# Kernel optimization log

Measured on AMD Instinct MI355X. Metric: run time of the kernel, lower is better.

The kernel has to match this reference:

```python
import jax, jax.numpy as jnp
import numpy as np

UNITS = 256
LB = -17.0
UB = 8.0
STEP = 0.05
NUM_BUCKETS = int((UB - LB) / STEP) + 1  # 501
RESIDUE = LB - STEP
W_INIT = 0.5
BATCH = 65536


def setup_inputs() -> dict:
    key = jax.random.key(0)
    kx, = jax.random.split(key, 1)
    x = jax.random.normal(kx, (BATCH, UNITS), dtype=jnp.float32)
    v = jnp.ones((UNITS, NUM_BUCKETS), dtype=jnp.float32) * W_INIT
    b = jnp.zeros((UNITS,), dtype=jnp.float32)
    return {"x": x, "v": v, "b": b}


def reference(x, v, b):
    # x: (batch, units); v: (units, num_buckets); b: (units,)
    x_clipped = jnp.clip(x, LB + 1e-9, UB - 1e-9)
    indx = ((x_clipped - LB + STEP) / STEP).astype(jnp.int32)
    indx = jnp.clip(indx, 0, NUM_BUCKETS - 1)  # (batch, units)
    delta = x_clipped - LB + STEP - indx.astype(x.dtype) * STEP

    w = jax.nn.relu(v)  # (units, num_buckets)
    # exclusive cumsum over buckets: csum[u, j] = sum_{k<j} w[u, k]
    csum = jnp.cumsum(w, axis=1)
    csum = jnp.concatenate([jnp.zeros((w.shape[0], 1), w.dtype), csum[:, :-1]], axis=1)

    unit_idx = jnp.arange(UNITS)[None, :]  # (1, units) broadcasts with indx
    csum_g = csum[unit_idx, indx]  # (batch, units)
    w_g = w[unit_idx, indx]        # (batch, units)

    # Equivalent to sum over buckets of (triangular step mask + scattered delta) * relu(v)
    logits = STEP * csum_g + delta * w_g + RESIDUE + b[None, :]
    return jax.nn.sigmoid(logits)
```

## Files before the change

kernel.cpp:

```cpp
#include <hip/hip_runtime.h>

#define UNITS 256
#define NB 501
#define NBA 502
#define STEPF 0.05f
#define LBF -17.0f
#define UBF 8.0f
#define RESIDUEF -17.05f
#define LOG2E 1.4426950408889634f

#define WLO 208
#define WSZ 224
#define UPB 32
#define PADF 225
#define THREADS 1024
#define ROWS_PB 2048
#define CHUNKS 16
#define RD 3

typedef float floatx4 __attribute__((ext_vector_type(4)));

__global__ __launch_bounds__(256) void build_table_kernel(
    const float* __restrict__ v, const float* __restrict__ b,
    float* __restrict__ gtab) {
  const int lane = threadIdx.x & 63;
  const int wave = threadIdx.x >> 6;
  const int u = blockIdx.x * 4 + wave;
  if (u >= UNITS) return;

  const float* vu = v + u * NB;
  float pref[8];
  float run = 0.0f;
#pragma unroll
  for (int k = 0; k < 8; ++k) {
    const int j = lane * 8 + k;
    const float wv = (j < NB) ? fmaxf(vu[j], 0.0f) : 0.0f;
    pref[k] = run;
    run += wv;
  }
  float s = run;
#pragma unroll
  for (int d = 1; d < 64; d <<= 1) {
    const float o = __shfl_up(s, d, 64);
    if (lane >= d) s += o;
  }
  const float base = s - run;
  const float off = RESIDUEF + b[u];
#pragma unroll
  for (int k = 0; k < 8; ++k) {
    const int j = lane * 8 + k;
    if (j < NBA) {
      gtab[u * NBA + j] = (STEPF * (base + pref[k]) + off) * LOG2E;
    }
  }
}

__global__ __launch_bounds__(THREADS, 8) void iso_main_kernel(
    const float* __restrict__ x, const float* __restrict__ gtab,
    float* __restrict__ out) {
  __shared__ float tab[UPB * PADF];

  const int bu = blockIdx.x & 7;
  const int bb = blockIdx.x >> 3;
  const int u0 = bu * UPB;
  const int tid = threadIdx.x;

  {
    const int ul = tid >> 5;
    const int jt = tid & 31;
    const float* __restrict__ src = gtab + (u0 + ul) * NBA + WLO;
    float* __restrict__ dst = tab + ul * PADF;
#pragma unroll
    for (int r = 0; r < 7; ++r) {
      const int j = jt + r * 32;
      dst[j] = src[j];
    }
    if (jt == 0) dst[224] = src[224];
  }

  const int rowoff = tid >> 3;
  const int col4 = tid & 7;
  const floatx4* __restrict__ x4 = reinterpret_cast<const floatx4*>(x);
  floatx4* __restrict__ o4 = reinterpret_cast<floatx4*>(out);
  const int g0 = (bb * ROWS_PB + rowoff) * (UNITS / 4) + bu * (UPB / 4) + col4;
  const int gstep = 128 * (UNITS / 4);
  const int qrow = col4 * 4;

  __syncthreads();

  floatx4 xv[4];
#pragma unroll
  for (int c = 0; c < RD; ++c) xv[c] = x4[g0 + c * gstep];
  __builtin_amdgcn_sched_barrier(0);

#pragma unroll
  for (int c = 0; c < CHUNKS; ++c) {
    if (c + RD < CHUNKS)
      xv[(c + RD) & 3] = x4[g0 + (c + RD) * gstep];
    __builtin_amdgcn_sched_barrier(0);

    const floatx4 cur = xv[c & 3];
    const float xs[4] = {cur.x, cur.y, cur.z, cur.w};
    float os[4];
#pragma unroll
    for (int k = 0; k < 4; ++k) {
      const float xc = fminf(fmaxf(xs[k], LBF + 1e-9f), UBF - 1e-9f);
      const float t = xc - LBF + STEPF;
      const float ft = t * 20.0f;
      const int idx = (int)ft;
      const float f = ft - (float)idx;
      const unsigned iw = (unsigned)(idx - WLO);
      float a0, a1;
      if (iw < WSZ) {
        const float* p = &tab[(qrow + k) * PADF + (int)iw];
        a0 = p[0];
        a1 = p[1];
      } else {
        const int ci = idx < 1 ? 1 : (idx > NB - 1 ? NB - 1 : idx);
        const float* g = gtab + (u0 + qrow + k) * NBA + ci;
        a0 = g[0];
        a1 = g[1];
      }
      const float l2 = fmaf(f, a1 - a0, a0);
      const float e = __builtin_amdgcn_exp2f(-l2);
      os[k] = __builtin_amdgcn_rcpf(1.0f + e);
    }
    floatx4 ov;
    ov.x = os[0]; ov.y = os[1]; ov.z = os[2]; ov.w = os[3];
    __builtin_nontemporal_store(ov, &o4[g0 + c * gstep]);
    __builtin_amdgcn_sched_barrier(0);
  }
}

extern "C" void kernel_launch(void* const* d_in, const int* in_sizes, int n_in,
                              void* d_out, int out_size, void* d_ws,
                              size_t ws_size, hipStream_t stream) {
  const float* x = (const float*)d_in[0];
  const float* v = (const float*)d_in[1];
  const float* b = (const float*)d_in[2];
  float* out = (float*)d_out;
  float* gtab = (float*)d_ws;

  build_table_kernel<<<64, 256, 0, stream>>>(v, b, gtab);

  const int rows = out_size / UNITS;
  const int grid = (UNITS / UPB) * (rows / ROWS_PB);
  iso_main_kernel<<<grid, THREADS, 0, stream>>>(x, gtab, out);
}
```

Baseline: 131.7 us.

## Fuse table build into main kernel with full per-unit LDS table

Drops the separate table-building kernel. Each block now computes the prefix-sum logit table for its 32 units directly into shared memory, holding the full 502-entry table instead of a 224-entry window with a global fallback, which removes the branch and the global gather. Rows per block are halved to 1024 and the x prefetch depth is raised, with the first x loads issued before the barrier so they overlap table construction. In exchange every block recomputes the table from v, shared memory per block roughly doubles, and the grid doubles.

```diff
diff --git a/kernel.cpp b/kernel.cpp
--- a/kernel.cpp
+++ b/kernel.cpp
@@ -9,73 +9,57 @@
 #define RESIDUEF -17.05f
 #define LOG2E 1.4426950408889634f
 
-#define WLO 208
-#define WSZ 224
 #define UPB 32
-#define PADF 225
+#define PADF 503
 #define THREADS 1024
-#define ROWS_PB 2048
-#define CHUNKS 16
-#define RD 3
+#define ROWS_PB 1024
+#define CHUNKS 8
+#define RD 5
 
 typedef float floatx4 __attribute__((ext_vector_type(4)));
 
-__global__ __launch_bounds__(256) void build_table_kernel(
-    const float* __restrict__ v, const float* __restrict__ b,
-    float* __restrict__ gtab) {
-  const int lane = threadIdx.x & 63;
-  const int wave = threadIdx.x >> 6;
-  const int u = blockIdx.x * 4 + wave;
-  if (u >= UNITS) return;
-
-  const float* vu = v + u * NB;
-  float pref[8];
-  float run = 0.0f;
-#pragma unroll
-  for (int k = 0; k < 8; ++k) {
-    const int j = lane * 8 + k;
-    const float wv = (j < NB) ? fmaxf(vu[j], 0.0f) : 0.0f;
-    pref[k] = run;
-    run += wv;
-  }
-  float s = run;
-#pragma unroll
-  for (int d = 1; d < 64; d <<= 1) {
-    const float o = __shfl_up(s, d, 64);
-    if (lane >= d) s += o;
-  }
-  const float base = s - run;
-  const float off = RESIDUEF + b[u];
-#pragma unroll
-  for (int k = 0; k < 8; ++k) {
-    const int j = lane * 8 + k;
-    if (j < NBA) {
-      gtab[u * NBA + j] = (STEPF * (base + pref[k]) + off) * LOG2E;
-    }
-  }
-}
-
 __global__ __launch_bounds__(THREADS, 8) void iso_main_kernel(
-    const float* __restrict__ x, const float* __restrict__ gtab,
-    float* __restrict__ out) {
+    const float* __restrict__ x, const float* __restrict__ v,
+    const float* __restrict__ b, float* __restrict__ out) {
   __shared__ float tab[UPB * PADF];
 
   const int bu = blockIdx.x & 7;
   const int bb = blockIdx.x >> 3;
   const int u0 = bu * UPB;
   const int tid = threadIdx.x;
+  const int lane = tid & 63;
+  const int wv = tid >> 6;
 
-  {
-    const int ul = tid >> 5;
-    const int jt = tid & 31;
-    const float* __restrict__ src = gtab + (u0 + ul) * NBA + WLO;
+#pragma unroll
+  for (int r = 0; r < 2; ++r) {
+    const int ul = wv * 2 + r;
+    const int u = u0 + ul;
+    const float* __restrict__ vu = v + u * NB;
+    float pref[8];
+    float run = 0.0f;
+#pragma unroll
+    for (int k = 0; k < 8; ++k) {
+      const int j = lane * 8 + k;
+      const float wvv = (j < NB) ? fmaxf(vu[j], 0.0f) : 0.0f;
+      pref[k] = run;
+      run += wvv;
+    }
+    float s = run;
+#pragma unroll
+    for (int d = 1; d < 64; d <<= 1) {
+      const float o = __shfl_up(s, d, 64);
+      if (lane >= d) s += o;
+    }
+    const float base = s - run;
+    const float off = RESIDUEF + b[u];
     float* __restrict__ dst = tab + ul * PADF;
 #pragma unroll
-    for (int r = 0; r < 7; ++r) {
-      const int j = jt + r * 32;
-      dst[j] = src[j];
+    for (int k = 0; k < 8; ++k) {
+      const int j = lane * 8 + k;
+      if (j < NBA) {
+        dst[j] = (STEPF * (base + pref[k]) + off) * LOG2E;
+      }
     }
-    if (jt == 0) dst[224] = src[224];
   }
 
   const int rowoff = tid >> 3;
@@ -86,20 +70,19 @@
   const int gstep = 128 * (UNITS / 4);
   const int qrow = col4 * 4;
 
+  floatx4 xv[8];
+#pragma unroll
+  for (int c = 0; c < RD; ++c) xv[c & 7] = x4[g0 + c * gstep];
+  __builtin_amdgcn_sched_barrier(0);
   __syncthreads();
-
-  floatx4 xv[4];
-#pragma unroll
-  for (int c = 0; c < RD; ++c) xv[c] = x4[g0 + c * gstep];
-  __builtin_amdgcn_sched_barrier(0);
 
 #pragma unroll
   for (int c = 0; c < CHUNKS; ++c) {
     if (c + RD < CHUNKS)
-      xv[(c + RD) & 3] = x4[g0 + (c + RD) * gstep];
+      xv[(c + RD) & 7] = x4[g0 + (c + RD) * gstep];
     __builtin_amdgcn_sched_barrier(0);
 
-    const floatx4 cur = xv[c & 3];
+    const floatx4 cur = xv[c & 7];
     const float xs[4] = {cur.x, cur.y, cur.z, cur.w};
     float os[4];
 #pragma unroll
@@ -107,20 +90,12 @@
       const float xc = fminf(fmaxf(xs[k], LBF + 1e-9f), UBF - 1e-9f);
       const float t = xc - LBF + STEPF;
       const float ft = t * 20.0f;
-      const int idx = (int)ft;
+      int idx = (int)ft;
+      idx = idx > NB - 1 ? NB - 1 : idx;
       const float f = ft - (float)idx;
-      const unsigned iw = (unsigned)(idx - WLO);
-      float a0, a1;
-      if (iw < WSZ) {
-        const float* p = &tab[(qrow + k) * PADF + (int)iw];
-        a0 = p[0];
-        a1 = p[1];
-      } else {
-        const int ci = idx < 1 ? 1 : (idx > NB - 1 ? NB - 1 : idx);
-        const float* g = gtab + (u0 + qrow + k) * NBA + ci;
-        a0 = g[0];
-        a1 = g[1];
-      }
+      const float* p = &tab[(qrow + k) * PADF + idx];
+      const float a0 = p[0];
+      const float a1 = p[1];
       const float l2 = fmaf(f, a1 - a0, a0);
       const float e = __builtin_amdgcn_exp2f(-l2);
       os[k] = __builtin_amdgcn_rcpf(1.0f + e);
@@ -139,11 +114,8 @@
   const float* v = (const float*)d_in[1];
   const float* b = (const float*)d_in[2];
   float* out = (float*)d_out;
-  float* gtab = (float*)d_ws;
-
-  build_table_kernel<<<64, 256, 0, stream>>>(v, b, gtab);
 
   const int rows = out_size / UNITS;
   const int grid = (UNITS / UPB) * (rows / ROWS_PB);
-  iso_main_kernel<<<grid, THREADS, 0, stream>>>(x, gtab, out);
+  iso_main_kernel<<<grid, THREADS, 0, stream>>>(x, v, b, out);
 }
```

Result: no change. 129.3 us (-1.9%).
